# Kernel optimization log

Measured on AMD Instinct MI355X. Metric: run time of the kernel, lower is better.

Reference implementation:

```python
import jax, jax.numpy as jnp
import numpy as np

N_NODES = 10000
N_EDGES = 320000
K = 5
C_IN = 128
C_OUT = 128


def setup_inputs() -> dict:
    key = jax.random.key(0)
    k_h, k_x, k_w, k_b = jax.random.split(key, 4)
    h = jax.random.normal(k_h, (N_NODES, C_IN), dtype=jnp.float32)
    X = jax.random.normal(k_x, (N_EDGES, K), dtype=jnp.float32)
    weight = jax.random.normal(k_w, (K, C_IN, C_OUT), dtype=jnp.float32) * 0.05
    bias = jax.random.normal(k_b, (C_OUT,), dtype=jnp.float32)
    # Unique (src, dst) pairs so scatter-set == segment-sum (matches torch indexing assignment).
    rng = np.random.default_rng(0)
    lin = np.unique(rng.integers(0, N_NODES * N_NODES, size=int(N_EDGES * 1.3)))
    assert len(lin) >= N_EDGES
    lin = lin[:N_EDGES]
    edge_index = jnp.asarray(np.stack([lin // N_NODES, lin % N_NODES]), dtype=jnp.int64)
    batch_node = jnp.zeros((N_NODES,), dtype=jnp.float32)
    return {"h": h, "X": X, "edge_index": edge_index, "batch_node": batch_node,
            "weight": weight, "bias": bias}


def reference(h, X, edge_index, batch_node, weight, bias):
    # Original torch code scatters X.T into a dense (K, N, N) adjacency and does
    # res = A @ h; that equals, per order k:
    #   res[k, i, :] = sum_{e: src_e = i} X[e, k] * h[dst_e, :]
    # which we compute sparsely with segment_sum (edges are unique).
    N = h.shape[0]
    src = edge_index[0]
    dst = edge_index[1]
    h_dst = h[dst]  # [E, C_in] gathered destination features

    def per_k(xk):  # xk: [E] edge values for one order k
        return jax.ops.segment_sum(xk[:, None] * h_dst, src, num_segments=N)  # [N, C_in]

    res_k = jax.vmap(per_k, in_axes=1)(X)  # [K, N, C_in]
    out = jnp.einsum('kni,kio->no', res_k, weight) + bias  # [N, C_out]
    return out
```

## Files before the change

kernel.cpp:

```cpp
#include <hip/hip_runtime.h>

#define N_NODES 10000
#define N_EDGES 320000
#define KDIM 640
#define C_OUT 128

typedef __attribute__((ext_vector_type(8))) short short8;
typedef __attribute__((ext_vector_type(4))) float floatx4;

__device__ __forceinline__ unsigned short f2bf(float f) {
    unsigned int b = __float_as_uint(f);
    b = (b + 0x7FFFu + ((b >> 16) & 1u)) >> 16;
    return (unsigned short)b;
}
__device__ __forceinline__ unsigned int pack2(float x, float y) {
    return (unsigned int)f2bf(x) | ((unsigned int)f2bf(y) << 16);
}
__device__ __forceinline__ float2 unpack2(unsigned int u) {
    float2 r;
    r.x = __uint_as_float(u << 16);
    r.y = __uint_as_float(u & 0xFFFF0000u);
    return r;
}

__global__ __launch_bounds__(256) void prep(
        const float* __restrict__ h, uint2* __restrict__ hb4,
        const float* __restrict__ W, unsigned short* __restrict__ Wt,
        const int* __restrict__ src, int* __restrict__ offsets) {
    const int bid = blockIdx.x;
    const int tid = threadIdx.x;

    if (bid < 1250) {
        const int t = bid * 256 + tid;
        float4 v = ((const float4*)h)[t];
        uint2 o;
        o.x = pack2(v.x, v.y);
        o.y = pack2(v.z, v.w);
        hb4[t] = o;
    } else if (bid < 1330) {
        __shared__ float tile[32][33];
        const int b = bid - 1250;
        const int k0 = (b % 20) * 32, o0 = (b / 20) * 32;
        const int tx = tid & 31, ty = tid >> 5;
#pragma unroll
        for (int i = 0; i < 4; ++i)
            tile[ty + 8 * i][tx] = W[(size_t)(k0 + ty + 8 * i) * C_OUT + o0 + tx];
        __syncthreads();
#pragma unroll
        for (int i = 0; i < 4; ++i)
            Wt[(size_t)(o0 + ty + 8 * i) * KDIM + k0 + tx] = f2bf(tile[tx][ty + 8 * i]);
    } else {
        const int n = (bid - 1330) * 256 + tid;
        if (n > N_NODES) return;
        int lo = 0, hi = N_EDGES;
        while (lo < hi) {
            int mid = (lo + hi) >> 1;
            if (src[mid] < n) lo = mid + 1; else hi = mid;
        }
        offsets[n] = lo;
    }
}

__global__ __launch_bounds__(512, 4) void fused_spectconv(
        const uint2* __restrict__ h4,
        const float* __restrict__ X,
        const int* __restrict__ dst,
        const int* __restrict__ offsets,
        const unsigned short* __restrict__ Wt,
        const float* __restrict__ bias,
        float* __restrict__ out) {
    __shared__ unsigned short Rs[16][648];

    const int tid  = threadIdx.x;
    const int wv   = tid >> 6;
    const int lane = tid & 63;
    const int slot = lane >> 5;
    const int l    = lane & 31;
    const int m0   = blockIdx.x * 16;

    for (int nn = 0; nn < 2; ++nn) {
        const int node = m0 + wv * 2 + nn;
        float a0x=0,a0y=0,a0z=0,a0w=0, a1x=0,a1y=0,a1z=0,a1w=0,
              a2x=0,a2y=0,a2z=0,a2w=0, a3x=0,a3y=0,a3z=0,a3w=0,
              a4x=0,a4y=0,a4z=0,a4w=0;

        const int e0 = offsets[node];
        const int e1 = offsets[node + 1];

        for (int base = e0; base < e1; base += 64) {
            const int cnt = min(64, e1 - base);
            const int le  = base + ((lane < cnt) ? lane : (cnt - 1));
            const int dv  = dst[le];
            const float* Xp = X + (size_t)le * 5;
            const float xk0 = Xp[0], xk1 = Xp[1], xk2 = Xp[2],
                        xk3 = Xp[3], xk4 = Xp[4];
            const int nsteps = (cnt + 1) >> 1;

#pragma unroll 2
            for (int j = 0; j < nsteps; ++j) {
                const int  ew    = 2 * j + slot;
                const bool valid = (ew < cnt);
                const int  ewc   = valid ? ew : (cnt - 1);
                const int  d     = __shfl(dv, ewc);
                const uint2 u    = h4[(size_t)d * 32 + l];
                float b0 = __shfl(xk0, ewc), b1 = __shfl(xk1, ewc),
                      b2 = __shfl(xk2, ewc), b3 = __shfl(xk3, ewc),
                      b4 = __shfl(xk4, ewc);
                b0 = valid ? b0 : 0.f;  b1 = valid ? b1 : 0.f;
                b2 = valid ? b2 : 0.f;  b3 = valid ? b3 : 0.f;
                b4 = valid ? b4 : 0.f;
                const float2 lo = unpack2(u.x), hi = unpack2(u.y);
                a0x = fmaf(b0, lo.x, a0x); a0y = fmaf(b0, lo.y, a0y);
                a0z = fmaf(b0, hi.x, a0z); a0w = fmaf(b0, hi.y, a0w);
                a1x = fmaf(b1, lo.x, a1x); a1y = fmaf(b1, lo.y, a1y);
                a1z = fmaf(b1, hi.x, a1z); a1w = fmaf(b1, hi.y, a1w);
                a2x = fmaf(b2, lo.x, a2x); a2y = fmaf(b2, lo.y, a2y);
                a2z = fmaf(b2, hi.x, a2z); a2w = fmaf(b2, hi.y, a2w);
                a3x = fmaf(b3, lo.x, a3x); a3y = fmaf(b3, lo.y, a3y);
                a3z = fmaf(b3, hi.x, a3z); a3w = fmaf(b3, hi.y, a3w);
                a4x = fmaf(b4, lo.x, a4x); a4y = fmaf(b4, lo.y, a4y);
                a4z = fmaf(b4, hi.x, a4z); a4w = fmaf(b4, hi.y, a4w);
            }
        }

        a0x += __shfl(a0x, lane ^ 32); a0y += __shfl(a0y, lane ^ 32);
        a0z += __shfl(a0z, lane ^ 32); a0w += __shfl(a0w, lane ^ 32);
        a1x += __shfl(a1x, lane ^ 32); a1y += __shfl(a1y, lane ^ 32);
        a1z += __shfl(a1z, lane ^ 32); a1w += __shfl(a1w, lane ^ 32);
        a2x += __shfl(a2x, lane ^ 32); a2y += __shfl(a2y, lane ^ 32);
        a2z += __shfl(a2z, lane ^ 32); a2w += __shfl(a2w, lane ^ 32);
        a3x += __shfl(a3x, lane ^ 32); a3y += __shfl(a3y, lane ^ 32);
        a3z += __shfl(a3z, lane ^ 32); a3w += __shfl(a3w, lane ^ 32);
        a4x += __shfl(a4x, lane ^ 32); a4y += __shfl(a4y, lane ^ 32);
        a4z += __shfl(a4z, lane ^ 32); a4w += __shfl(a4w, lane ^ 32);

        if (lane < 32) {
            const int nrel = wv * 2 + nn;
            uint2 w0; w0.x = pack2(a0x, a0y); w0.y = pack2(a0z, a0w);
            uint2 w1; w1.x = pack2(a1x, a1y); w1.y = pack2(a1z, a1w);
            uint2 w2; w2.x = pack2(a2x, a2y); w2.y = pack2(a2z, a2w);
            uint2 w3; w3.x = pack2(a3x, a3y); w3.y = pack2(a3z, a3w);
            uint2 w4; w4.x = pack2(a4x, a4y); w4.y = pack2(a4z, a4w);
            *(uint2*)&Rs[nrel][0 * 128 + 4 * l] = w0;
            *(uint2*)&Rs[nrel][1 * 128 + 4 * l] = w1;
            *(uint2*)&Rs[nrel][2 * 128 + 4 * l] = w2;
            *(uint2*)&Rs[nrel][3 * 128 + 4 * l] = w3;
            *(uint2*)&Rs[nrel][4 * 128 + 4 * l] = w4;
        }
    }

    __syncthreads();

    const int col  = lane & 15;
    const int quad = lane >> 4;
    const int c0   = wv * 16;

    floatx4 acc = {0.f, 0.f, 0.f, 0.f};
    const unsigned short* wrow = Wt + (size_t)(c0 + col) * KDIM + quad * 8;

#pragma unroll
    for (int kc = 0; kc < 20; ++kc) {
        const short8 af = *(const short8*)&Rs[col][kc * 32 + quad * 8];
        const short8 bf = *(const short8*)(wrow + kc * 32);
        acc = __builtin_amdgcn_mfma_f32_16x16x32_bf16(af, bf, acc, 0, 0, 0);
    }

    const float bv = bias[c0 + col];
#pragma unroll
    for (int r = 0; r < 4; ++r) {
        const int m = m0 + quad * 4 + r;
        out[(size_t)m * C_OUT + c0 + col] = acc[r] + bv;
    }
}

extern "C" void kernel_launch(void* const* d_in, const int* in_sizes, int n_in,
                              void* d_out, int out_size, void* d_ws, size_t ws_size,
                              hipStream_t stream) {
    const float* h      = (const float*)d_in[0];
    const float* X      = (const float*)d_in[1];
    const int*   ei     = (const int*)d_in[2];
    const float* weight = (const float*)d_in[4];
    const float* bias   = (const float*)d_in[5];
    float* out = (float*)d_out;

    const int* src = ei;
    const int* dst = ei + N_EDGES;

    char* wsb = (char*)d_ws;
    int*            offsets = (int*)wsb;
    uint2*          hb4     = (uint2*)(wsb + (64 << 10));
    unsigned short* Wtb     = (unsigned short*)(wsb + (64 << 10) + (4 << 20));

    prep<<<1370, 256, 0, stream>>>(h, hb4, weight, Wtb, src, offsets);
    fused_spectconv<<<625, 512, 0, stream>>>(hb4, X, dst, offsets, Wtb, bias, out);
}
```

Baseline: 112.1 us.

## Assign one node per half-wave and drop cross-half reduction and shuffles

Each half-wavefront now processes its own node, looping over that node's edges directly. Edge indices and X values are read with uniform per-half loads instead of being staged through lane-wide loads and shuffles, and the final cross-half shuffle reduction is removed. This cuts shuffle and reduction overhead and processes two nodes concurrently per wave. The cost is divergence between the two halves when their nodes have different degrees, plus redundant per-lane scalar loads of dst and X.

```diff
diff --git a/kernel.cpp b/kernel.cpp
--- a/kernel.cpp
+++ b/kernel.cpp
@@ -78,75 +78,49 @@
     const int l    = lane & 31;
     const int m0   = blockIdx.x * 16;
 
-    for (int nn = 0; nn < 2; ++nn) {
-        const int node = m0 + wv * 2 + nn;
-        float a0x=0,a0y=0,a0z=0,a0w=0, a1x=0,a1y=0,a1z=0,a1w=0,
-              a2x=0,a2y=0,a2z=0,a2w=0, a3x=0,a3y=0,a3z=0,a3w=0,
-              a4x=0,a4y=0,a4z=0,a4w=0;
+    const int node = m0 + wv * 2 + slot;
 
-        const int e0 = offsets[node];
-        const int e1 = offsets[node + 1];
+    float a0x=0,a0y=0,a0z=0,a0w=0, a1x=0,a1y=0,a1z=0,a1w=0,
+          a2x=0,a2y=0,a2z=0,a2w=0, a3x=0,a3y=0,a3z=0,a3w=0,
+          a4x=0,a4y=0,a4z=0,a4w=0;
 
-        for (int base = e0; base < e1; base += 64) {
-            const int cnt = min(64, e1 - base);
-            const int le  = base + ((lane < cnt) ? lane : (cnt - 1));
-            const int dv  = dst[le];
-            const float* Xp = X + (size_t)le * 5;
-            const float xk0 = Xp[0], xk1 = Xp[1], xk2 = Xp[2],
-                        xk3 = Xp[3], xk4 = Xp[4];
-            const int nsteps = (cnt + 1) >> 1;
+    const int e0 = offsets[node];
+    const int e1 = offsets[node + 1];
 
-#pragma unroll 2
-            for (int j = 0; j < nsteps; ++j) {
-                const int  ew    = 2 * j + slot;
-                const bool valid = (ew < cnt);
-                const int  ewc   = valid ? ew : (cnt - 1);
-                const int  d     = __shfl(dv, ewc);
-                const uint2 u    = h4[(size_t)d * 32 + l];
-                float b0 = __shfl(xk0, ewc), b1 = __shfl(xk1, ewc),
-                      b2 = __shfl(xk2, ewc), b3 = __shfl(xk3, ewc),
-                      b4 = __shfl(xk4, ewc);
-                b0 = valid ? b0 : 0.f;  b1 = valid ? b1 : 0.f;
-                b2 = valid ? b2 : 0.f;  b3 = valid ? b3 : 0.f;
-                b4 = valid ? b4 : 0.f;
-                const float2 lo = unpack2(u.x), hi = unpack2(u.y);
-                a0x = fmaf(b0, lo.x, a0x); a0y = fmaf(b0, lo.y, a0y);
-                a0z = fmaf(b0, hi.x, a0z); a0w = fmaf(b0, hi.y, a0w);
-                a1x = fmaf(b1, lo.x, a1x); a1y = fmaf(b1, lo.y, a1y);
-                a1z = fmaf(b1, hi.x, a1z); a1w = fmaf(b1, hi.y, a1w);
-                a2x = fmaf(b2, lo.x, a2x); a2y = fmaf(b2, lo.y, a2y);
-                a2z = fmaf(b2, hi.x, a2z); a2w = fmaf(b2, hi.y, a2w);
-                a3x = fmaf(b3, lo.x, a3x); a3y = fmaf(b3, lo.y, a3y);
-                a3z = fmaf(b3, hi.x, a3z); a3w = fmaf(b3, hi.y, a3w);
-                a4x = fmaf(b4, lo.x, a4x); a4y = fmaf(b4, lo.y, a4y);
-                a4z = fmaf(b4, hi.x, a4z); a4w = fmaf(b4, hi.y, a4w);
-            }
-        }
+#pragma unroll 4
+    for (int e = e0; e < e1; ++e) {
+        const int d = dst[e];
+        const float x0 = X[(size_t)e * 5 + 0];
+        const float x1 = X[(size_t)e * 5 + 1];
+        const float x2 = X[(size_t)e * 5 + 2];
+        const float x3 = X[(size_t)e * 5 + 3];
+        const float x4 = X[(size_t)e * 5 + 4];
+        const uint2 u  = h4[(size_t)d * 32 + l];
+        const float2 lo = unpack2(u.x), hi = unpack2(u.y);
+        a0x = fmaf(x0, lo.x, a0x); a0y = fmaf(x0, lo.y, a0y);
+        a0z = fmaf(x0, hi.x, a0z); a0w = fmaf(x0, hi.y, a0w);
+        a1x = fmaf(x1, lo.x, a1x); a1y = fmaf(x1, lo.y, a1y);
+        a1z = fmaf(x1, hi.x, a1z); a1w = fmaf(x1, hi.y, a1w);
+        a2x = fmaf(x2, lo.x, a2x); a2y = fmaf(x2, lo.y, a2y);
+        a2z = fmaf(x2, hi.x, a2z); a2w = fmaf(x2, hi.y, a2w);
+        a3x = fmaf(x3, lo.x, a3x); a3y = fmaf(x3, lo.y, a3y);
+        a3z = fmaf(x3, hi.x, a3z); a3w = fmaf(x3, hi.y, a3w);
+        a4x = fmaf(x4, lo.x, a4x); a4y = fmaf(x4, lo.y, a4y);
+        a4z = fmaf(x4, hi.x, a4z); a4w = fmaf(x4, hi.y, a4w);
+    }
 
-        a0x += __shfl(a0x, lane ^ 32); a0y += __shfl(a0y, lane ^ 32);
-        a0z += __shfl(a0z, lane ^ 32); a0w += __shfl(a0w, lane ^ 32);
-        a1x += __shfl(a1x, lane ^ 32); a1y += __shfl(a1y, lane ^ 32);
-        a1z += __shfl(a1z, lane ^ 32); a1w += __shfl(a1w, lane ^ 32);
-        a2x += __shfl(a2x, lane ^ 32); a2y += __shfl(a2y, lane ^ 32);
-        a2z += __shfl(a2z, lane ^ 32); a2w += __shfl(a2w, lane ^ 32);
-        a3x += __shfl(a3x, lane ^ 32); a3y += __shfl(a3y, lane ^ 32);
-        a3z += __shfl(a3z, lane ^ 32); a3w += __shfl(a3w, lane ^ 32);
-        a4x += __shfl(a4x, lane ^ 32); a4y += __shfl(a4y, lane ^ 32);
-        a4z += __shfl(a4z, lane ^ 32); a4w += __shfl(a4w, lane ^ 32);
-
-        if (lane < 32) {
-            const int nrel = wv * 2 + nn;
-            uint2 w0; w0.x = pack2(a0x, a0y); w0.y = pack2(a0z, a0w);
-            uint2 w1; w1.x = pack2(a1x, a1y); w1.y = pack2(a1z, a1w);
-            uint2 w2; w2.x = pack2(a2x, a2y); w2.y = pack2(a2z, a2w);
-            uint2 w3; w3.x = pack2(a3x, a3y); w3.y = pack2(a3z, a3w);
-            uint2 w4; w4.x = pack2(a4x, a4y); w4.y = pack2(a4z, a4w);
-            *(uint2*)&Rs[nrel][0 * 128 + 4 * l] = w0;
-            *(uint2*)&Rs[nrel][1 * 128 + 4 * l] = w1;
-            *(uint2*)&Rs[nrel][2 * 128 + 4 * l] = w2;
-            *(uint2*)&Rs[nrel][3 * 128 + 4 * l] = w3;
-            *(uint2*)&Rs[nrel][4 * 128 + 4 * l] = w4;
-        }
+    {
+        const int nrel = wv * 2 + slot;
+        uint2 w0; w0.x = pack2(a0x, a0y); w0.y = pack2(a0z, a0w);
+        uint2 w1; w1.x = pack2(a1x, a1y); w1.y = pack2(a1z, a1w);
+        uint2 w2; w2.x = pack2(a2x, a2y); w2.y = pack2(a2z, a2w);
+        uint2 w3; w3.x = pack2(a3x, a3y); w3.y = pack2(a3z, a3w);
+        uint2 w4; w4.x = pack2(a4x, a4y); w4.y = pack2(a4z, a4w);
+        *(uint2*)&Rs[nrel][0 * 128 + 4 * l] = w0;
+        *(uint2*)&Rs[nrel][1 * 128 + 4 * l] = w1;
+        *(uint2*)&Rs[nrel][2 * 128 + 4 * l] = w2;
+        *(uint2*)&Rs[nrel][3 * 128 + 4 * l] = w3;
+        *(uint2*)&Rs[nrel][4 * 128 + 4 * l] = w4;
     }
 
     __syncthreads();
```

Measured after the change: 107.4 us. 1.04x faster.
